# Kernel optimization log

Hardware: AMD Instinct MI355X
Metric: run time of the kernel (lower is better)

The kernel has to match this reference:

```python
import jax, jax.numpy as jnp
import numpy as np

B = 2        # batch size
G = 128      # dense grid extent per axis
N = 200000   # occupied voxels
M = 200000   # query points
C = 128      # feature dim
IGNORE = -1  # ignore_label

# 8 trilinear corner offsets [8,3]
_OFFSETS = jnp.array([[i, j, k] for i in (0, 1) for j in (0, 1) for k in (0, 1)], dtype=jnp.int32)


def setup_inputs() -> dict:
    key = jax.random.key(0)
    k1, k2, k3, k4, k5 = jax.random.split(key, 5)
    xyz = jax.random.randint(k1, (N, 3), 0, G).astype(jnp.int32)
    bids = jnp.sort(jax.random.randint(k2, (N,), 0, B)).astype(jnp.int32)  # sorted batch ids (sparse tensor layout)
    coords = jnp.concatenate([bids[:, None], xyz], axis=1)                 # [N,4]
    features_3d = jax.random.normal(k3, (N, C), dtype=jnp.float32)
    qxyz = jax.random.uniform(k4, (M, 3), minval=0.0, maxval=float(G - 1))
    qb = jnp.sort(jax.random.randint(k5, (M,), 0, B)).astype(jnp.float32)
    query_points = jnp.concatenate([qb[:, None], qxyz], axis=1)            # [M,4]
    return {"features_3d": features_3d, "coords": coords, "query_points": query_points}


def _trilinear(features_3d, coords, query_points):
    bids = coords[:, 0]
    # per-batch coordinate shift (torch.amin per batch)
    shift = jax.ops.segment_min(coords[:, 1:], bids, num_segments=B)       # [B,3]
    c = coords[:, 1:] - shift[bids]                                        # [N,3]
    qb = query_points[:, 0].astype(jnp.int32)                              # [M]
    q = query_points[:, 1:] - shift[qb].astype(query_points.dtype)         # [M,3]

    # dense occupancy grid: voxel row index, IGNORE where empty
    occ = jnp.full((B, G, G, G), IGNORE, dtype=jnp.int32)
    occ = occ.at[bids, c[:, 0], c[:, 1], c[:, 2]].set(jnp.arange(N, dtype=jnp.int32))

    base = jnp.floor(q).astype(jnp.int32)                                  # [M,3]
    frac = q - base.astype(q.dtype)                                        # [M,3]
    corner = base[:, None, :] + _OFFSETS[None]                             # [M,8,3]
    # trilinear weights: prod over dims of frac (offset=1) or 1-frac (offset=0)
    w = jnp.prod(jnp.where(_OFFSETS[None] == 1, frac[:, None, :], 1.0 - frac[:, None, :]), axis=-1)  # [M,8]

    in_bounds = jnp.all((corner >= 0) & (corner < G), axis=-1)             # [M,8]
    cc = jnp.clip(corner, 0, G - 1)
    idx = occ[qb[:, None], cc[..., 0], cc[..., 1], cc[..., 2]]             # [M,8]
    valid = in_bounds & (idx != IGNORE)

    interp_idx = jnp.where(valid, idx, IGNORE)                             # [M,8]
    interp_w = jnp.where(valid, w, 0.0).astype(features_3d.dtype)          # [M,8]

    gathered = features_3d[jnp.maximum(interp_idx, 0)]                     # [M,8,C]
    query_features = jnp.einsum('mk,mkc->mc', interp_w, gathered)          # [M,C]

    # per-voxel accumulated interpolation weight (invalid -> segment N, dropped)
    seg = jnp.where(valid, interp_idx, N).reshape(-1)
    accum_voxel_weights = jax.ops.segment_sum(interp_w.reshape(-1), seg, num_segments=N + 1)[:N]
    return query_features, interp_idx, interp_w, accum_voxel_weights


def reference(features_3d, coords, query_points):
    return _trilinear(features_3d, coords, query_points)
```

## Files before the change

### kernel.cpp

```cpp
#include <hip/hip_runtime.h>

#define NB   2
#define GG   128
#define CC   128
#define QPB  64

typedef float v4f __attribute__((ext_vector_type(4)));

constexpr int OCC_INTS = NB * GG * GG * GG;

__global__ void __launch_bounds__(256)
init_kernel(int* __restrict__ occ, float* __restrict__ acc,
            int* __restrict__ shift, int n) {
    const int tid = blockIdx.x * 256 + threadIdx.x;
    const int nth = gridDim.x * 256;
    if (tid < NB * 3) shift[tid] = 0x7FFFFFFF;
    int4* occ4 = (int4*)occ;
    for (int i = tid; i < OCC_INTS / 4; i += nth)
        occ4[i] = make_int4(-1, -1, -1, -1);
    for (int i = tid; i < n; i += nth) acc[i] = 0.0f;
}

__global__ void __launch_bounds__(256)
scatter_kernel(const int4* __restrict__ coords, int* __restrict__ shift,
               int* __restrict__ occ, int n) {
    __shared__ int smin[NB * 3];
    if (threadIdx.x < NB * 3) smin[threadIdx.x] = 0x7FFFFFFF;
    __syncthreads();
    for (int i = blockIdx.x * 256 + threadIdx.x; i < n; i += gridDim.x * 256) {
        const int4 c = coords[i];
        atomicMin(&smin[c.x * 3 + 0], c.y);
        atomicMin(&smin[c.x * 3 + 1], c.z);
        atomicMin(&smin[c.x * 3 + 2], c.w);
        atomicMax(&occ[((c.x * GG + c.y) * GG + c.z) * GG + c.w], i);
    }
    __syncthreads();
    if (threadIdx.x < NB * 3) atomicMin(&shift[threadIdx.x], smin[threadIdx.x]);
}

__global__ void __launch_bounds__(256)
query_kernel(const float* __restrict__ feats,
             const v4f* __restrict__ qpts,
             const int* __restrict__ shift,
             const int* __restrict__ occ,
             float* __restrict__ out_qf,
             float* __restrict__ out_idx,
             float* __restrict__ out_w,
             float* __restrict__ out_acc, int mq) {
    __shared__ int   s_idx[QPB][8];
    __shared__ float s_w[QPB][8];
    const int tid   = threadIdx.x;
    const int qbase = blockIdx.x * QPB;

    if (tid < QPB) {
        const int gq = qbase + tid;
        int   lidx[8];
        float lw[8];
#pragma unroll
        for (int cn = 0; cn < 8; ++cn) { lidx[cn] = -1; lw[cn] = 0.0f; }
        if (gq < mq) {
            const v4f qp = qpts[gq];
            const int qb = (int)qp.x;
            const int s0 = shift[qb * 3 + 0], s1 = shift[qb * 3 + 1],
                      s2 = shift[qb * 3 + 2];
            const float q0 = qp.y - (float)s0, q1 = qp.z - (float)s1,
                        q2 = qp.w - (float)s2;
            const float b0 = floorf(q0), b1 = floorf(q1), b2 = floorf(q2);
            const float f0 = q0 - b0, f1 = q1 - b1, f2 = q2 - b2;
            const int i0 = (int)b0, i1 = (int)b1, i2 = (int)b2;
            const int u0 = i0 + s0, u1 = i1 + s1, u2 = i2 + s2;
#pragma unroll
            for (int cn = 0; cn < 8; ++cn) {
                const int oi = (cn >> 2) & 1, oj = (cn >> 1) & 1, ok = cn & 1;
                const int c0 = i0 + oi, c1 = i1 + oj, c2 = i2 + ok;
                const int a0 = u0 + oi, a1 = u1 + oj, a2 = u2 + ok;
                const float w = (oi ? f0 : 1.0f - f0) *
                                (oj ? f1 : 1.0f - f1) *
                                (ok ? f2 : 1.0f - f2);
                const bool inb = c0 >= 0 && c0 < GG && c1 >= 0 && c1 < GG &&
                                 c2 >= 0 && c2 < GG &&
                                 a0 < GG && a1 < GG && a2 < GG;
                int idx = -1;
                if (inb) idx = occ[((qb * GG + a0) * GG + a1) * GG + a2];
                const float fw = (idx != -1) ? w : 0.0f;
                lidx[cn] = idx;
                lw[cn]   = fw;
                if (idx >= 0 && fw != 0.0f) atomicAdd(&out_acc[idx], fw);
            }
            const v4f vi0 = {(float)lidx[0], (float)lidx[1], (float)lidx[2], (float)lidx[3]};
            const v4f vi1 = {(float)lidx[4], (float)lidx[5], (float)lidx[6], (float)lidx[7]};
            const v4f vw0 = {lw[0], lw[1], lw[2], lw[3]};
            const v4f vw1 = {lw[4], lw[5], lw[6], lw[7]};
            __builtin_nontemporal_store(vi0, (v4f*)&out_idx[(size_t)gq * 8]);
            __builtin_nontemporal_store(vi1, (v4f*)&out_idx[(size_t)gq * 8 + 4]);
            __builtin_nontemporal_store(vw0, (v4f*)&out_w[(size_t)gq * 8]);
            __builtin_nontemporal_store(vw1, (v4f*)&out_w[(size_t)gq * 8 + 4]);
        }
#pragma unroll
        for (int cn = 0; cn < 8; ++cn) {
            s_idx[tid][cn] = lidx[cn];
            s_w[tid][cn]   = lw[cn];
        }
    }
    __syncthreads();

    const int lane = tid & 31;
    const int qsub = tid >> 5;
    const int c4   = lane << 2;
#pragma unroll
    for (int p = 0; p < 8; ++p) {
        const int q  = p * 8 + qsub;
        const int gq = qbase + q;
        if (gq >= mq) continue;
        v4f acc = {0.0f, 0.0f, 0.0f, 0.0f};
#pragma unroll
        for (int k = 0; k < 8; ++k) {
            const int idx = s_idx[q][k];
            if (idx >= 0) {
                const float w = s_w[q][k];
                const v4f f = *(const v4f*)&feats[(size_t)idx * CC + c4];
                acc += w * f;
            }
        }
        __builtin_nontemporal_store(acc, (v4f*)&out_qf[(size_t)gq * CC + c4]);
    }
}

extern "C" void kernel_launch(void* const* d_in, const int* in_sizes, int n_in,
                              void* d_out, int out_size, void* d_ws, size_t ws_size,
                              hipStream_t stream) {
    const float* feats  = (const float*)d_in[0];
    const int4*  coords = (const int4*)d_in[1];
    const v4f*   qpts   = (const v4f*)d_in[2];

    const int n  = in_sizes[1] / 4;
    const int mq = in_sizes[2] / 4;

    float* out     = (float*)d_out;
    float* out_qf  = out;
    float* out_idx = out_qf  + (size_t)mq * CC;
    float* out_w   = out_idx + (size_t)mq * 8;
    float* out_acc = out_w   + (size_t)mq * 8;

    int* shift = (int*)d_ws;
    int* occ   = (int*)((char*)d_ws + 256);

    init_kernel   <<<2048, 256, 0, stream>>>(occ, out_acc, shift, n);
    scatter_kernel<<<(n + 255) / 256, 256, 0, stream>>>(coords, shift, occ, n);
    query_kernel  <<<(mq + QPB - 1) / QPB, 256, 0, stream>>>(
        feats, qpts, shift, occ, out_qf, out_idx, out_w, out_acc, mq);
}
```

Measured before the change: 66.48 us.

## Spread corner lookups over all threads and compact valid neighbors via ballot

```diff
diff --git a/kernel.cpp b/kernel.cpp
--- a/kernel.cpp
+++ b/kernel.cpp
@@ -3,7 +3,8 @@
 #define NB   2
 #define GG   128
 #define CC   128
-#define QPB  64
+#define QPB  32
+#define BLK  256
 
 typedef float v4f __attribute__((ext_vector_type(4)));
 
@@ -47,82 +48,71 @@
              float* __restrict__ out_idx,
              float* __restrict__ out_w,
              float* __restrict__ out_acc, int mq) {
-    __shared__ int   s_idx[QPB][8];
-    __shared__ float s_w[QPB][8];
+    __shared__ int  s_cnt[QPB];
+    __shared__ int2 s_pair[QPB][8];
     const int tid   = threadIdx.x;
     const int qbase = blockIdx.x * QPB;
+    const int q     = tid >> 3;
+    const int cn    = tid & 7;
+    const int gq    = qbase + q;
 
-    if (tid < QPB) {
-        const int gq = qbase + tid;
-        int   lidx[8];
-        float lw[8];
-#pragma unroll
-        for (int cn = 0; cn < 8; ++cn) { lidx[cn] = -1; lw[cn] = 0.0f; }
-        if (gq < mq) {
-            const v4f qp = qpts[gq];
-            const int qb = (int)qp.x;
-            const int s0 = shift[qb * 3 + 0], s1 = shift[qb * 3 + 1],
-                      s2 = shift[qb * 3 + 2];
-            const float q0 = qp.y - (float)s0, q1 = qp.z - (float)s1,
-                        q2 = qp.w - (float)s2;
-            const float b0 = floorf(q0), b1 = floorf(q1), b2 = floorf(q2);
-            const float f0 = q0 - b0, f1 = q1 - b1, f2 = q2 - b2;
-            const int i0 = (int)b0, i1 = (int)b1, i2 = (int)b2;
-            const int u0 = i0 + s0, u1 = i1 + s1, u2 = i2 + s2;
-#pragma unroll
-            for (int cn = 0; cn < 8; ++cn) {
-                const int oi = (cn >> 2) & 1, oj = (cn >> 1) & 1, ok = cn & 1;
-                const int c0 = i0 + oi, c1 = i1 + oj, c2 = i2 + ok;
-                const int a0 = u0 + oi, a1 = u1 + oj, a2 = u2 + ok;
-                const float w = (oi ? f0 : 1.0f - f0) *
-                                (oj ? f1 : 1.0f - f1) *
-                                (ok ? f2 : 1.0f - f2);
-                const bool inb = c0 >= 0 && c0 < GG && c1 >= 0 && c1 < GG &&
-                                 c2 >= 0 && c2 < GG &&
-                                 a0 < GG && a1 < GG && a2 < GG;
-                int idx = -1;
-                if (inb) idx = occ[((qb * GG + a0) * GG + a1) * GG + a2];
-                const float fw = (idx != -1) ? w : 0.0f;
-                lidx[cn] = idx;
-                lw[cn]   = fw;
-                if (idx >= 0 && fw != 0.0f) atomicAdd(&out_acc[idx], fw);
-            }
-            const v4f vi0 = {(float)lidx[0], (float)lidx[1], (float)lidx[2], (float)lidx[3]};
-            const v4f vi1 = {(float)lidx[4], (float)lidx[5], (float)lidx[6], (float)lidx[7]};
-            const v4f vw0 = {lw[0], lw[1], lw[2], lw[3]};
-            const v4f vw1 = {lw[4], lw[5], lw[6], lw[7]};
-            __builtin_nontemporal_store(vi0, (v4f*)&out_idx[(size_t)gq * 8]);
-            __builtin_nontemporal_store(vi1, (v4f*)&out_idx[(size_t)gq * 8 + 4]);
-            __builtin_nontemporal_store(vw0, (v4f*)&out_w[(size_t)gq * 8]);
-            __builtin_nontemporal_store(vw1, (v4f*)&out_w[(size_t)gq * 8 + 4]);
-        }
-#pragma unroll
-        for (int cn = 0; cn < 8; ++cn) {
-            s_idx[tid][cn] = lidx[cn];
-            s_w[tid][cn]   = lw[cn];
-        }
+    int   idx = -1;
+    float fw  = 0.0f;
+    if (gq < mq) {
+        const v4f qp = qpts[gq];
+        const int qb = (int)qp.x;
+        const int s0 = shift[qb * 3 + 0], s1 = shift[qb * 3 + 1],
+                  s2 = shift[qb * 3 + 2];
+        const float q0 = qp.y - (float)s0, q1 = qp.z - (float)s1,
+                    q2 = qp.w - (float)s2;
+        const float b0 = floorf(q0), b1 = floorf(q1), b2 = floorf(q2);
+        const float f0 = q0 - b0, f1 = q1 - b1, f2 = q2 - b2;
+        const int i0 = (int)b0, i1 = (int)b1, i2 = (int)b2;
+        const int oi = (cn >> 2) & 1, oj = (cn >> 1) & 1, ok = cn & 1;
+        const int c0 = i0 + oi, c1 = i1 + oj, c2 = i2 + ok;
+        const int a0 = c0 + s0, a1 = c1 + s1, a2 = c2 + s2;
+        const float w = (oi ? f0 : 1.0f - f0) *
+                        (oj ? f1 : 1.0f - f1) *
+                        (ok ? f2 : 1.0f - f2);
+        const bool inb = c0 >= 0 && c0 < GG && c1 >= 0 && c1 < GG &&
+                         c2 >= 0 && c2 < GG &&
+                         a0 < GG && a1 < GG && a2 < GG;
+        const int p0 = min(max(a0, 0), GG - 1);
+        const int p1 = min(max(a1, 0), GG - 1);
+        const int p2 = min(max(a2, 0), GG - 1);
+        int v = occ[((qb * GG + p0) * GG + p1) * GG + p2];
+        idx = inb ? v : -1;
+        fw  = (idx != -1) ? w : 0.0f;
+
+        out_idx[(size_t)gq * 8 + cn] = (float)idx;
+        out_w[(size_t)gq * 8 + cn]   = fw;
+        if (idx >= 0 && fw != 0.0f) atomicAdd(&out_acc[idx], fw);
     }
+
+    const unsigned long long bal = __ballot(idx >= 0);
+    const int lane = tid & 63;
+    const unsigned grp = (unsigned)((bal >> (lane & 56)) & 0xFFull);
+    const int pos = __popc(grp & ((1u << (lane & 7)) - 1u));
+    if (idx >= 0) s_pair[q][pos] = make_int2(idx, __float_as_int(fw));
+    if (cn == 0) s_cnt[q] = __popc(grp);
     __syncthreads();
 
-    const int lane = tid & 31;
-    const int qsub = tid >> 5;
-    const int c4   = lane << 2;
+    const int sg = tid >> 5;
+    const int c4 = (tid & 31) << 2;
 #pragma unroll
-    for (int p = 0; p < 8; ++p) {
-        const int q  = p * 8 + qsub;
-        const int gq = qbase + q;
-        if (gq >= mq) continue;
+    for (int p = 0; p < 4; ++p) {
+        const int qq  = p * 8 + sg;
+        const int gq2 = qbase + qq;
+        if (gq2 >= mq) continue;
+        const int cnt = s_cnt[qq];
         v4f acc = {0.0f, 0.0f, 0.0f, 0.0f};
-#pragma unroll
-        for (int k = 0; k < 8; ++k) {
-            const int idx = s_idx[q][k];
-            if (idx >= 0) {
-                const float w = s_w[q][k];
-                const v4f f = *(const v4f*)&feats[(size_t)idx * CC + c4];
-                acc += w * f;
-            }
+        for (int j = 0; j < cnt; ++j) {
+            const int2  pr = s_pair[qq][j];
+            const float w  = __int_as_float(pr.y);
+            const v4f   f  = *(const v4f*)&feats[(size_t)pr.x * CC + c4];
+            acc += w * f;
         }
-        __builtin_nontemporal_store(acc, (v4f*)&out_qf[(size_t)gq * CC + c4]);
+        __builtin_nontemporal_store(acc, (v4f*)&out_qf[(size_t)gq2 * CC + c4]);
     }
 }
 
@@ -147,6 +137,6 @@
 
     init_kernel   <<<2048, 256, 0, stream>>>(occ, out_acc, shift, n);
     scatter_kernel<<<(n + 255) / 256, 256, 0, stream>>>(coords, shift, occ, n);
-    query_kernel  <<<(mq + QPB - 1) / QPB, 256, 0, stream>>>(
+    query_kernel  <<<(mq + QPB - 1) / QPB, BLK, 0, stream>>>(
         feats, qpts, shift, occ, out_qf, out_idx, out_w, out_acc, mq);
 }
```

After: 63.54 us. -4.4%, faster.
